# Performance work log

Measured on AMD Instinct MI355X. Metric: run time of the kernel, lower is better.

Reference implementation:

```python
import jax, jax.numpy as jnp
import numpy as np

EPS = 1e-8

def _div(n, d):
    # div_with_small_value: d = d if d > eps else eps
    return n / jnp.where(d > EPS, d, EPS)

def _lstm_dir(x, Wih, Whh, bih, bhh):
    # x: (B, L, I) -> (hs (B, L, H), h_last (B, H))
    B, L, _ = x.shape
    H = Whh.shape[1]
    xg = jnp.einsum('bli,gi->blg', x, Wih) + bih + bhh  # (B, L, 4H)
    def step(carry, g):
        h, c = carry
        g = g + h @ Whh.T
        i, f, gg, o = jnp.split(g, 4, axis=-1)
        c = jax.nn.sigmoid(f) * c + jax.nn.sigmoid(i) * jnp.tanh(gg)
        h = jax.nn.sigmoid(o) * jnp.tanh(c)
        return (h, c), h
    init = (jnp.zeros((B, H), x.dtype), jnp.zeros((B, H), x.dtype))
    (hT, _), hs = jax.lax.scan(step, init, jnp.swapaxes(xg, 0, 1))
    return jnp.swapaxes(hs, 0, 1), hT

def _bilstm(x, pf, pb):
    fw, fwT = _lstm_dir(x, *pf)
    bw_r, bwT = _lstm_dir(x[:, ::-1], *pb)
    return fw, bw_r[:, ::-1], fwT, bwT

def _mp_full(v1, v2, w):
    # v1 (B,L,H); v2 (B,H) or (B,L,H); w (P,H) -> (B,L,P)
    wv1 = v1[:, :, None, :] * w                      # (B,L,P,H)
    if v2.ndim == 2:
        wv2 = v2[:, None, None, :] * w               # (B,1,P,H)
    else:
        wv2 = v2[:, :, None, :] * w                  # (B,L,P,H)
    num = jnp.sum(wv1 * wv2, -1)
    den = jnp.linalg.norm(wv1, axis=-1) * jnp.linalg.norm(wv2, axis=-1)
    return num / jnp.maximum(den, EPS)               # torch cosine_similarity eps

def _mp_pairwise(v1, v2, w):
    # v1 (B,L1,H), v2 (B,L2,H), w (P,H) -> (B,L1,L2,P)
    wv1 = w[None, :, None, :] * v1[:, None]          # (B,P,L1,H)
    wv2 = w[None, :, None, :] * v2[:, None]          # (B,P,L2,H)
    n = jnp.einsum('bpld,bpmd->bplm', wv1, wv2)
    d = jnp.linalg.norm(wv1, axis=-1)[..., :, None] * jnp.linalg.norm(wv2, axis=-1)[..., None, :]
    return jnp.transpose(_div(n, d), (0, 2, 3, 1))

def _attention(v1, v2):
    # cosine similarity matrix (B, L1, L2)
    n = jnp.einsum('bld,bmd->blm', v1, v2)
    d = jnp.linalg.norm(v1, axis=-1)[:, :, None] * jnp.linalg.norm(v2, axis=-1)[:, None, :]
    return _div(n, d)

def _forward(emb, cWih_f, cWhh_f, cbih_f, cbhh_f, cWih_b, cWhh_b, cbih_b, cbhh_b,
             aWih_f, aWhh_f, abih_f, abhh_f, aWih_b, aWhh_b, abih_b, abhh_b,
             mp_w1, mp_w2, mp_w3, mp_w4, mp_w5, mp_w6, mp_w7, mp_w8,
             fc1_W, fc1_b, fc2_W, fc2_b, text_a, text_b):
    p = emb[text_a]
    h = emb[text_b]
    cpf_p = (cWih_f, cWhh_f, cbih_f, cbhh_f)
    cpb_p = (cWih_b, cWhh_b, cbih_b, cbhh_b)
    con_p_fw, con_p_bw, _, _ = _bilstm(p, cpf_p, cpb_p)
    con_h_fw, con_h_bw, _, _ = _bilstm(h, cpf_p, cpb_p)
    # full matching
    mv_p_full_fw = _mp_full(con_p_fw, con_h_fw[:, -1], mp_w1)
    mv_p_full_bw = _mp_full(con_p_bw, con_h_bw[:, 0], mp_w2)
    mv_h_full_fw = _mp_full(con_h_fw, con_p_fw[:, -1], mp_w1)
    mv_h_full_bw = _mp_full(con_h_bw, con_p_bw[:, 0], mp_w2)
    # maxpool matching
    mv_max_fw = _mp_pairwise(con_p_fw, con_h_fw, mp_w3)
    mv_max_bw = _mp_pairwise(con_p_bw, con_h_bw, mp_w4)
    mv_p_max_fw = mv_max_fw.max(2); mv_p_max_bw = mv_max_bw.max(2)
    mv_h_max_fw = mv_max_fw.max(1); mv_h_max_bw = mv_max_bw.max(1)
    # attentive matching
    att_fw = _attention(con_p_fw, con_h_fw)          # (B,L1,L2)
    att_bw = _attention(con_p_bw, con_h_bw)
    att_h_fw = con_h_fw[:, None] * att_fw[..., None]     # (B,L1,L2,H)
    att_h_bw = con_h_bw[:, None] * att_bw[..., None]
    att_p_fw = con_p_fw[:, :, None] * att_fw[..., None]  # (B,L1,L2,H)
    att_p_bw = con_p_bw[:, :, None] * att_bw[..., None]
    att_mean_h_fw = _div(att_h_fw.sum(2), att_fw.sum(2, keepdims=True))
    att_mean_h_bw = _div(att_h_bw.sum(2), att_bw.sum(2, keepdims=True))
    att_mean_p_fw = _div(att_p_fw.sum(1), jnp.swapaxes(att_fw.sum(1, keepdims=True), 1, 2))
    att_mean_p_bw = _div(att_p_bw.sum(1), jnp.swapaxes(att_bw.sum(1, keepdims=True), 1, 2))
    mv_p_att_mean_fw = _mp_full(con_p_fw, att_mean_h_fw, mp_w5)
    mv_p_att_mean_bw = _mp_full(con_p_bw, att_mean_h_bw, mp_w6)
    mv_h_att_mean_fw = _mp_full(con_h_fw, att_mean_p_fw, mp_w5)
    mv_h_att_mean_bw = _mp_full(con_h_bw, att_mean_p_bw, mp_w6)
    att_max_h_fw = att_h_fw.max(2); att_max_h_bw = att_h_bw.max(2)
    att_max_p_fw = att_p_fw.max(1); att_max_p_bw = att_p_bw.max(1)
    mv_p_att_max_fw = _mp_full(con_p_fw, att_max_h_fw, mp_w7)
    mv_p_att_max_bw = _mp_full(con_p_bw, att_max_h_bw, mp_w8)
    mv_h_att_max_fw = _mp_full(con_h_fw, att_max_p_fw, mp_w7)
    mv_h_att_max_bw = _mp_full(con_h_bw, att_max_p_bw, mp_w8)
    mv_p = jnp.concatenate([mv_p_full_fw, mv_p_max_fw, mv_p_att_mean_fw, mv_p_att_max_fw,
                            mv_p_full_bw, mv_p_max_bw, mv_p_att_mean_bw, mv_p_att_max_bw], 2)
    mv_h = jnp.concatenate([mv_h_full_fw, mv_h_max_fw, mv_h_att_mean_fw, mv_h_att_max_fw,
                            mv_h_full_bw, mv_h_max_bw, mv_h_att_mean_bw, mv_h_att_max_bw], 2)
    apf = (aWih_f, aWhh_f, abih_f, abhh_f)
    apb = (aWih_b, aWhh_b, abih_b, abhh_b)
    _, _, p_fwT, p_bwT = _bilstm(mv_p, apf, apb)
    _, _, h_fwT, h_bwT = _bilstm(mv_h, apf, apb)
    x = jnp.concatenate([p_fwT, p_bwT, h_fwT, h_bwT], 1)  # (B, 4H)
    x = jnp.tanh(x @ fc1_W.T + fc1_b)
    return x @ fc2_W.T + fc2_b

def setup_inputs() -> dict:
    key = jax.random.key(0)
    ks = jax.random.split(key, 40)
    B, L, V, E, H, P = 16, 128, 30000, 300, 128, 4
    def n(i, shape, s=0.05):
        return jax.random.normal(ks[i], shape, jnp.float32) * s
    inp = {
        'text_a': jax.random.randint(ks[0], (B, L), 0, V, jnp.int32),
        'text_b': jax.random.randint(ks[1], (B, L), 0, V, jnp.int32),
        'emb': n(2, (V, E), 0.1),
        'cWih_f': n(3, (4*H, E)), 'cWhh_f': n(4, (4*H, H)), 'cbih_f': n(5, (4*H,)), 'cbhh_f': n(6, (4*H,)),
        'cWih_b': n(7, (4*H, E)), 'cWhh_b': n(8, (4*H, H)), 'cbih_b': n(9, (4*H,)), 'cbhh_b': n(10, (4*H,)),
        'aWih_f': n(11, (4*H, 8*P)), 'aWhh_f': n(12, (4*H, H)), 'abih_f': n(13, (4*H,)), 'abhh_f': n(14, (4*H,)),
        'aWih_b': n(15, (4*H, 8*P)), 'aWhh_b': n(16, (4*H, H)), 'abih_b': n(17, (4*H,)), 'abhh_b': n(18, (4*H,)),
        'fc1_W': n(19, (2*H, 4*H)), 'fc1_b': n(20, (2*H,)),
        'fc2_W': n(21, (2, 2*H)), 'fc2_b': n(22, (2,)),
    }
    for i in range(1, 9):
        inp[f'mp_w{i}'] = jax.random.uniform(ks[22 + i], (P, H), jnp.float32)
    return inp

def reference(text_a, text_b, emb, cWih_f, cWhh_f, cbih_f, cbhh_f, cWih_b, cWhh_b, cbih_b, cbhh_b,
              aWih_f, aWhh_f, abih_f, abhh_f, aWih_b, aWhh_b, abih_b, abhh_b,
              fc1_W, fc1_b, fc2_W, fc2_b, mp_w1, mp_w2, mp_w3, mp_w4, mp_w5, mp_w6, mp_w7, mp_w8):
    return _forward(emb, cWih_f, cWhh_f, cbih_f, cbhh_f, cWih_b, cWhh_b, cbih_b, cbhh_b,
                    aWih_f, aWhh_f, abih_f, abhh_f, aWih_b, aWhh_b, abih_b, abhh_b,
                    mp_w1, mp_w2, mp_w3, mp_w4, mp_w5, mp_w6, mp_w7, mp_w8,
                    fc1_W, fc1_b, fc2_W, fc2_b, text_a, text_b)
```

## Files before the change

### kernel.cpp

```cpp
#include <hip/hip_runtime.h>

#define B_ 16
#define L_ 128
#define ML_ 2048
#define E_ 300
#define H_ 128
#define G_ 512
#define EPSV 1e-8f

typedef const float* fp;
typedef __attribute__((ext_vector_type(2))) float f32x2;

__device__ __forceinline__ float sigm(float x) { return 1.f / (1.f + __expf(-x)); }
__device__ __forceinline__ float tanh_f(float x) {
  float e = __expf(-2.f * fabsf(x));
  float r = (1.f - e) / (1.f + e);
  return copysignf(r, x);
}
__device__ __forceinline__ float ddiv(float n, float d) {
  return n / (d > EPSV ? d : EPSV);
}
__device__ __forceinline__ void pkfma(f32x2& d, f32x2 a, f32x2 b) {
  asm("v_pk_fma_f32 %0, %1, %2, %0" : "+v"(d) : "v"(a), "v"(b));
}

__global__ __launch_bounds__(256) void k_proj(
    fp __restrict__ emb,
    const int* __restrict__ ta, const int* __restrict__ tb,
    fp Wf, fp Wb, fp bihf, fp bhhf, fp bihb, fp bhhb,
    float* __restrict__ xg)
{
  const int z = blockIdx.z;
  const int* txt = (z >> 1) ? tb : ta;
  fp W = (z & 1) ? Wb : Wf;
  fp bih = (z & 1) ? bihb : bihf;
  fp bhh = (z & 1) ? bhhb : bhhf;
  float* out = xg + (size_t)z * ML_ * G_;
  const int m0 = blockIdx.x * 64, n0 = blockIdx.y * 64;
  __shared__ float As[12][64];
  __shared__ float Bs[12][64];
  __shared__ int rowidx[64];
  const int tid = threadIdx.x;
  if (tid < 64) rowidx[tid] = txt[m0 + tid];
  __syncthreads();
  const int tm = tid >> 4, tn = tid & 15;
  float acc[4][4] = {};
  for (int k0 = 0; k0 < 300; k0 += 12) {
    for (int i = tid; i < 768; i += 256) {
      int m = i / 12, k = i - m * 12;
      As[k][m] = emb[(size_t)rowidx[m] * 300 + k0 + k];
    }
    for (int i = tid; i < 768; i += 256) {
      int n = i / 12, k = i - n * 12;
      Bs[k][n] = W[(size_t)(n0 + n) * 300 + k0 + k];
    }
    __syncthreads();
    #pragma unroll
    for (int k = 0; k < 12; ++k) {
      float4 a = *(const float4*)&As[k][tm * 4];
      float4 bv = *(const float4*)&Bs[k][tn * 4];
      float aa[4] = {a.x, a.y, a.z, a.w};
      #pragma unroll
      for (int i = 0; i < 4; ++i) {
        acc[i][0] = fmaf(aa[i], bv.x, acc[i][0]);
        acc[i][1] = fmaf(aa[i], bv.y, acc[i][1]);
        acc[i][2] = fmaf(aa[i], bv.z, acc[i][2]);
        acc[i][3] = fmaf(aa[i], bv.w, acc[i][3]);
      }
    }
    __syncthreads();
  }
  float biasv[4];
  #pragma unroll
  for (int j = 0; j < 4; ++j)
    biasv[j] = bih[n0 + tn * 4 + j] + bhh[n0 + tn * 4 + j];
  #pragma unroll
  for (int i = 0; i < 4; ++i) {
    float* row = out + (size_t)(m0 + tm * 4 + i) * G_ + n0 + tn * 4;
    #pragma unroll
    for (int j = 0; j < 4; ++j) row[j] = acc[i][j] + biasv[j];
  }
}

__global__ __launch_bounds__(512, 2) void k_lstm(
    fp __restrict__ xg, fp Whhf, fp Whhb, float* __restrict__ out)
{
  const int b = blockIdx.x, z = blockIdx.y, dir = z & 1;
  fp Whh = dir ? Whhb : Whhf;
  fp __restrict__ xgz = xg + ((size_t)z * ML_ + (size_t)b * L_) * G_;
  float* __restrict__ outz = out + ((size_t)z * ML_ + (size_t)b * L_) * H_;
  const int tid = threadIdx.x;
  const int wv = tid >> 6, l = tid & 63;
  const int kh = l & 1, ph = (l >> 1) & 1, jj = l >> 2;
  const int j = wv * 16 + jj;
  const int rA = ph * H_ + j;
  const int rB = rA + 2 * H_;
  f32x2 wA[32], wB[32];
  {
    const float4* pA = (const float4*)(Whh + (size_t)rA * H_ + kh * 64);
    const float4* pB = (const float4*)(Whh + (size_t)rB * H_ + kh * 64);
    float4* dA = (float4*)wA; float4* dB = (float4*)wB;
    #pragma unroll
    for (int q = 0; q < 16; ++q) dA[q] = pA[q];
    #pragma unroll
    for (int q = 0; q < 16; ++q) dB[q] = pB[q];
  }
  __shared__ float hs[2][128];
  if (tid < 128) hs[0][tid] = 0.f;
  float c = 0.f;
  const int pos0 = dir ? (L_ - 1) : 0;
  float xvA = xgz[(size_t)pos0 * G_ + rA];
  float xvB = xgz[(size_t)pos0 * G_ + rB];
  __syncthreads();
  int cur = 0;
  for (int t = 0; t < L_; ++t) {
    const int pos = dir ? (L_ - 1 - t) : t;
    const int tnext = (t + 1 < L_) ? (t + 1) : t;
    const int posn = dir ? (L_ - 1 - tnext) : tnext;
    float xvA_n = xgz[(size_t)posn * G_ + rA];
    float xvB_n = xgz[(size_t)posn * G_ + rB];
    f32x2 accA0 = {0.f, 0.f}, accA1 = {0.f, 0.f};
    f32x2 accB0 = {0.f, 0.f}, accB1 = {0.f, 0.f};
    const float4* h4 = (const float4*)(&hs[cur][kh * 64]);
    #pragma unroll
    for (int q = 0; q < 16; ++q) {
      float4 hv = h4[q];
      f32x2 hlo; hlo.x = hv.x; hlo.y = hv.y;
      f32x2 hhi; hhi.x = hv.z; hhi.y = hv.w;
      pkfma(accA0, wA[2 * q],     hlo);
      pkfma(accA1, wA[2 * q + 1], hhi);
      pkfma(accB0, wB[2 * q],     hlo);
      pkfma(accB1, wB[2 * q + 1], hhi);
    }
    float aA = (accA0.x + accA0.y) + (accA1.x + accA1.y);
    float aB = (accB0.x + accB0.y) + (accB1.x + accB1.y);
    aA += __shfl_xor(aA, 1, 64);
    aB += __shfl_xor(aB, 1, 64);
    aA += xvA; aB += xvB;
    float actA = sigm(aA);
    float actB = ph ? sigm(aB) : tanh_f(aB);
    float exA = __shfl_xor(actA, 2, 64);
    float exB = __shfl_xor(actB, 2, 64);
    float iv = ph ? exA : actA;
    float fv = ph ? actA : exA;
    float gv = ph ? exB : actB;
    float ov = ph ? actB : exB;
    c = fmaf(fv, c, iv * gv);
    float hn = ov * tanh_f(c);
    const int nxt = cur ^ 1;
    if ((l & 3) == 0) {
      hs[nxt][j] = hn;
      outz[(size_t)pos * H_ + j] = hn;
    }
    asm volatile("s_waitcnt lgkmcnt(0)" ::: "memory");
    __builtin_amdgcn_s_barrier();
    cur = nxt; xvA = xvA_n; xvB = xvB_n;
  }
}

__global__ __launch_bounds__(256) void k_att(
    fp __restrict__ con, fp w3, fp w4,
    float* __restrict__ att, float* __restrict__ ameanh, float* __restrict__ amaxh,
    float* __restrict__ pcpart, float* __restrict__ mv)
{
  const int b = blockIdx.x, dir = blockIdx.y, lt = blockIdx.z;
  const int l0 = lt * 32;
  fp __restrict__ cp = con + ((size_t)dir * B_ + b) * L_ * H_;
  fp __restrict__ ch = con + ((size_t)(2 + dir) * B_ + b) * L_ * H_;
  fp w = dir ? w4 : w3;
  float* __restrict__ attg = att + ((size_t)dir * B_ + b) * L_ * L_;
  __shared__ float cps[32][132];
  __shared__ float chs[32][132];
  __shared__ float w2s[4][128];
  __shared__ float attb[32][33];
  __shared__ float pcb[4][32][33];
  __shared__ float n0l[32], nql[4][32], n0m[32], nqm[4][32], asum_s[32];
  const int tid = threadIdx.x;
  for (int i = tid; i < 512; i += 256) {
    float wv = w[i];
    w2s[i >> 7][i & 127] = wv * wv;
  }
  for (int i = tid; i < 4096; i += 256)
    cps[i >> 7][i & 127] = cp[(size_t)(l0 + (i >> 7)) * H_ + (i & 127)];
  __syncthreads();
  for (int d = tid; d < 160; d += 256) {
    int l = d / 5, q = d - l * 5;
    const float4* vr = (const float4*)&cps[l][0];
    float s = 0.f;
    if (q == 0) {
      #pragma unroll 8
      for (int h4 = 0; h4 < 32; ++h4) {
        float4 v = vr[h4];
        s += v.x*v.x + v.y*v.y + v.z*v.z + v.w*v.w;
      }
      n0l[l] = sqrtf(s);
    } else {
      const float4* wr = (const float4*)&w2s[q - 1][0];
      #pragma unroll 8
      for (int h4 = 0; h4 < 32; ++h4) {
        float4 v = vr[h4]; float4 ww = wr[h4];
        s += v.x*v.x*ww.x + v.y*v.y*ww.y + v.z*v.z*ww.z + v.w*v.w*ww.w;
      }
      nql[q - 1][l] = sqrtf(s);
    }
  }
  const int tl = tid >> 3, t8 = tid & 7;
  float amean_acc[16], amax_acc[16];
  #pragma unroll
  for (int i = 0; i < 16; ++i) { amean_acc[i] = 0.f; amax_acc[i] = -3.4e38f; }
  float asum_reg = 0.f;
  float pmax_reg = -3.4e38f;
  for (int mc = 0; mc < 4; ++mc) {
    __syncthreads();
    for (int i = tid; i < 4096; i += 256)
      chs[i >> 7][i & 127] = ch[(size_t)(mc * 32 + (i >> 7)) * H_ + (i & 127)];
    __syncthreads();
    for (int d = tid; d < 160; d += 256) {
      int m = d / 5, q = d - m * 5;
      const float4* vr = (const float4*)&chs[m][0];
      float s = 0.f;
      if (q == 0) {
        #pragma unroll 8
        for (int h4 = 0; h4 < 32; ++h4) {
          float4 v = vr[h4];
          s += v.x*v.x + v.y*v.y + v.z*v.z + v.w*v.w;
        }
        n0m[m] = sqrtf(s);
      } else {
        const float4* wr = (const float4*)&w2s[q - 1][0];
        #pragma unroll 8
        for (int h4 = 0; h4 < 32; ++h4) {
          float4 v = vr[h4]; float4 ww = wr[h4];
          s += v.x*v.x*ww.x + v.y*v.y*ww.y + v.z*v.z*ww.z + v.w*v.w*ww.w;
        }
        nqm[q - 1][m] = sqrtf(s);
      }
    }
    __syncthreads();
    float a0[4], ap0[4], ap1[4], ap2[4], ap3[4];
    #pragma unroll
    for (int mm = 0; mm < 4; ++mm) { a0[mm]=0.f; ap0[mm]=0.f; ap1[mm]=0.f; ap2[mm]=0.f; ap3[mm]=0.f; }
    #pragma unroll 4
    for (int h4 = 0; h4 < 32; ++h4) {
      const float4 av = *(const float4*)&cps[tl][h4 * 4];
      const float4 q0 = *(const float4*)&w2s[0][h4 * 4];
      const float4 q1 = *(const float4*)&w2s[1][h4 * 4];
      const float4 q2 = *(const float4*)&w2s[2][h4 * 4];
      const float4 q3 = *(const float4*)&w2s[3][h4 * 4];
      #pragma unroll
      for (int mm = 0; mm < 4; ++mm) {
        const float4 cv = *(const float4*)&chs[t8 * 4 + mm][h4 * 4];
        float px = av.x * cv.x, py = av.y * cv.y, pz = av.z * cv.z, pw = av.w * cv.w;
        a0[mm] += (px + py) + (pz + pw);
        ap0[mm] += px * q0.x + py * q0.y + pz * q0.z + pw * q0.w;
        ap1[mm] += px * q1.x + py * q1.y + pz * q1.z + pw * q1.w;
        ap2[mm] += px * q2.x + py * q2.y + pz * q2.z + pw * q2.w;
        ap3[mm] += px * q3.x + py * q3.y + pz * q3.z + pw * q3.w;
      }
    }
    #pragma unroll
    for (int mm = 0; mm < 4; ++mm) {
      const int m = t8 * 4 + mm;
      float attv = ddiv(a0[mm], n0l[tl] * n0m[m]);
      attb[tl][m] = attv;
      attg[(size_t)(l0 + tl) * L_ + mc * 32 + m] = attv;
      pcb[0][tl][m] = ddiv(ap0[mm], nql[0][tl] * nqm[0][m]);
      pcb[1][tl][m] = ddiv(ap1[mm], nql[1][tl] * nqm[1][m]);
      pcb[2][tl][m] = ddiv(ap2[mm], nql[2][tl] * nqm[2][m]);
      pcb[3][tl][m] = ddiv(ap3[mm], nql[3][tl] * nqm[3][m]);
    }
    __syncthreads();
    for (int mq = 0; mq < 32; ++mq) {
      float avv = attb[tl][mq];
      const float4* cr = (const float4*)&chs[mq][t8 * 16];
      #pragma unroll
      for (int i = 0; i < 4; ++i) {
        float4 cv = cr[i];
        float t0 = avv * cv.x, t1 = avv * cv.y, t2 = avv * cv.z, t3 = avv * cv.w;
        amean_acc[4*i+0] += t0; amax_acc[4*i+0] = fmaxf(amax_acc[4*i+0], t0);
        amean_acc[4*i+1] += t1; amax_acc[4*i+1] = fmaxf(amax_acc[4*i+1], t1);
        amean_acc[4*i+2] += t2; amax_acc[4*i+2] = fmaxf(amax_acc[4*i+2], t2);
        amean_acc[4*i+3] += t3; amax_acc[4*i+3] = fmaxf(amax_acc[4*i+3], t3);
      }
    }
    if (tid < 32) {
      float s = 0.f;
      for (int mq = 0; mq < 32; ++mq) s += attb[tid][mq];
      asum_reg += s;
    }
    if (tid < 128) {
      const int p = tid >> 5, q = tid & 31;
      float mx = pmax_reg;
      for (int mq = 0; mq < 32; ++mq) mx = fmaxf(mx, pcb[p][q][mq]);
      pmax_reg = mx;
      float mx2 = -3.4e38f;
      for (int lq = 0; lq < 32; ++lq) mx2 = fmaxf(mx2, pcb[p][lq][q]);
      pcpart[((((size_t)dir * B_ + b) * 4 + lt) * 4 + p) * L_ + mc * 32 + q] = mx2;
    }
    __syncthreads();
  }
  if (tid < 32) asum_s[tid] = asum_reg;
  __syncthreads();
  {
    float den = asum_s[tl]; den = (den > EPSV) ? den : EPSV;
    const size_t base = (((size_t)dir * B_ + b) * L_ + l0 + tl) * H_ + t8 * 16;
    #pragma unroll
    for (int i = 0; i < 16; ++i) {
      ameanh[base + i] = amean_acc[i] / den;
      amaxh[base + i] = amax_acc[i];
    }
  }
  if (tid < 128) {
    const int p = tid >> 5, lq = tid & 31;
    mv[(size_t)(b * L_ + l0 + lq) * 32 + (dir ? 20 : 4) + p] = pmax_reg;
  }
}

__global__ __launch_bounds__(256) void k_col(
    fp __restrict__ con, fp __restrict__ att,
    fp __restrict__ pcpart,
    float* __restrict__ ameanp, float* __restrict__ amaxp, float* __restrict__ mv)
{
  const int b = blockIdx.x, dir = blockIdx.y, mt = blockIdx.z;
  const int m0 = mt * 32;
  fp __restrict__ cp = con + ((size_t)dir * B_ + b) * L_ * H_;
  fp __restrict__ attg = att + ((size_t)dir * B_ + b) * L_ * L_;
  __shared__ float atts[128][33];
  __shared__ float cpc[32][132];
  __shared__ float asum_s[32];
  const int tid = threadIdx.x;
  for (int i = tid; i < 4096; i += 256)
    atts[i >> 5][i & 31] = attg[(size_t)(i >> 5) * L_ + m0 + (i & 31)];
  __syncthreads();
  if (tid < 32) {
    float s = 0.f;
    for (int l = 0; l < 128; ++l) s += atts[l][tid];
    asum_s[tid] = s;
  }
  const int tm = tid >> 3, t8 = tid & 7;
  float mean_acc[16], max_acc[16];
  #pragma unroll
  for (int i = 0; i < 16; ++i) { mean_acc[i] = 0.f; max_acc[i] = -3.4e38f; }
  for (int lc = 0; lc < 4; ++lc) {
    __syncthreads();
    for (int i = tid; i < 4096; i += 256)
      cpc[i >> 7][i & 127] = cp[(size_t)(lc * 32 + (i >> 7)) * H_ + (i & 127)];
    __syncthreads();
    for (int lq = 0; lq < 32; ++lq) {
      float avv = atts[lc * 32 + lq][tm];
      const float4* cr = (const float4*)&cpc[lq][t8 * 16];
      #pragma unroll
      for (int i = 0; i < 4; ++i) {
        float4 cv = cr[i];
        float t0 = avv * cv.x, t1 = avv * cv.y, t2 = avv * cv.z, t3 = avv * cv.w;
        mean_acc[4*i+0] += t0; max_acc[4*i+0] = fmaxf(max_acc[4*i+0], t0);
        mean_acc[4*i+1] += t1; max_acc[4*i+1] = fmaxf(max_acc[4*i+1], t1);
        mean_acc[4*i+2] += t2; max_acc[4*i+2] = fmaxf(max_acc[4*i+2], t2);
        mean_acc[4*i+3] += t3; max_acc[4*i+3] = fmaxf(max_acc[4*i+3], t3);
      }
    }
  }
  __syncthreads();
  {
    float den = asum_s[tm]; den = (den > EPSV) ? den : EPSV;
    const size_t base = (((size_t)dir * B_ + b) * L_ + m0 + tm) * H_ + t8 * 16;
    #pragma unroll
    for (int i = 0; i < 16; ++i) {
      ameanp[base + i] = mean_acc[i] / den;
      amaxp[base + i] = max_acc[i];
    }
  }
  if (tid < 128) {
    const int p = tid >> 5, mq = tid & 31;
    float mx = -3.4e38f;
    #pragma unroll
    for (int lt = 0; lt < 4; ++lt)
      mx = fmaxf(mx, pcpart[((((size_t)dir * B_ + b) * 4 + lt) * 4 + p) * L_ + m0 + mq]);
    mv[(size_t)(ML_ + b * L_ + m0 + mq) * 32 + (dir ? 20 : 4) + p] = mx;
  }
}

__global__ __launch_bounds__(256) void k_mv(
    fp __restrict__ con,
    fp __restrict__ ameanh, fp __restrict__ amaxh,
    fp __restrict__ ameanp, fp __restrict__ amaxp,
    fp w1, fp w2, fp w5, fp w6, fp w7, fp w8,
    float* __restrict__ mv)
{
  int idx = blockIdx.x * 256 + threadIdx.x;
  const int p = idx & 3; int t1 = idx >> 2;
  const int type = t1 % 3; int t2 = t1 / 3;
  const int dir = t2 & 1; int t3 = t2 >> 1;
  const int l = t3 & 127; int t4 = t3 >> 7;
  const int b = t4 & 15; const int side = t4 >> 4;
  const float* v1 = con + (((size_t)(side ? 2 : 0) + dir) * B_ + b) * L_ * H_ + (size_t)l * H_;
  const float* v2;
  if (type == 0) {
    v2 = con + (((size_t)(side ? 0 : 2) + dir) * B_ + b) * L_ * H_ + (size_t)(dir ? 0 : L_ - 1) * H_;
  } else {
    const float* base = (type == 1) ? (side ? ameanp : ameanh) : (side ? amaxp : amaxh);
    v2 = base + (((size_t)dir * B_ + b) * L_ + l) * H_;
  }
  fp w = (type == 0) ? (dir ? w2 : w1) : (type == 1) ? (dir ? w6 : w5) : (dir ? w8 : w7);
  w += p * H_;
  float num = 0.f, s1 = 0.f, s2 = 0.f;
  for (int h = 0; h < H_; ++h) {
    float wv = w[h];
    float a = v1[h] * wv, bb = v2[h] * wv;
    num = fmaf(a, bb, num);
    s1 = fmaf(a, a, s1);
    s2 = fmaf(bb, bb, s2);
  }
  float den = sqrtf(s1) * sqrtf(s2);
  int slot = (type == 0) ? (dir ? 16 : 0) + p : (type == 1) ? (dir ? 24 : 8) + p : (dir ? 28 : 12) + p;
  mv[((size_t)side * ML_ + b * L_ + l) * 32 + slot] = ddiv(num, den);
}

__global__ __launch_bounds__(256) void k_aggproj(
    fp __restrict__ mv,
    fp Wf, fp Wb, fp bihf, fp bhhf, fp bihb, fp bhhb,
    float* __restrict__ xg)
{
  const int z = blockIdx.y, side = z >> 1, dir = z & 1;
  fp W = dir ? Wb : Wf;
  fp bih = dir ? bihb : bihf;
  fp bhh = dir ? bhhb : bhhf;
  const int r0 = blockIdx.x * 8;
  const float* src = mv + ((size_t)side * ML_ + r0) * 32;
  float* out = xg + ((size_t)z * ML_ + r0) * G_;
  __shared__ float mvs[8][32];
  const int tid = threadIdx.x;
  mvs[tid >> 5][tid & 31] = src[tid];
  __syncthreads();
  float w0[32], w1v[32];
  {
    const float4* wp = (const float4*)(W + (size_t)tid * 32);
    #pragma unroll
    for (int q = 0; q < 8; ++q) {
      float4 u = wp[q];
      w0[4*q+0] = u.x; w0[4*q+1] = u.y; w0[4*q+2] = u.z; w0[4*q+3] = u.w;
    }
    const float4* wp2 = (const float4*)(W + (size_t)(tid + 256) * 32);
    #pragma unroll
    for (int q = 0; q < 8; ++q) {
      float4 u = wp2[q];
      w1v[4*q+0] = u.x; w1v[4*q+1] = u.y; w1v[4*q+2] = u.z; w1v[4*q+3] = u.w;
    }
  }
  float bias0 = bih[tid] + bhh[tid];
  float bias1 = bih[tid + 256] + bhh[tid + 256];
  for (int r = 0; r < 8; ++r) {
    float acc0 = bias0, acc1 = bias1;
    #pragma unroll
    for (int k = 0; k < 32; ++k) {
      float xv = mvs[r][k];
      acc0 = fmaf(w0[k], xv, acc0);
      acc1 = fmaf(w1v[k], xv, acc1);
    }
    out[(size_t)r * G_ + tid] = acc0;
    out[(size_t)r * G_ + tid + 256] = acc1;
  }
}

__global__ __launch_bounds__(256) void k_fc(
    fp __restrict__ aggseq,
    fp fc1W, fp fc1b, fp fc2W, fp fc2b,
    float* __restrict__ out)
{
  const int b = blockIdx.x, tid = threadIdx.x;
  __shared__ float x[512];
  __shared__ float y[256];
  for (int i = tid; i < 512; i += 256) {
    int z = i >> 7, h = i & 127;
    int l = (z & 1) ? 0 : (L_ - 1);
    x[i] = aggseq[(((size_t)z * B_ + b) * L_ + l) * H_ + h];
  }
  __syncthreads();
  {
    float acc = fc1b[tid];
    const float4* wr = (const float4*)(fc1W + (size_t)tid * 512);
    const float4* x4 = (const float4*)x;
    #pragma unroll 8
    for (int k4 = 0; k4 < 128; ++k4) {
      float4 u = wr[k4];
      float4 xv = x4[k4];
      acc = fmaf(u.x, xv.x, acc);
      acc = fmaf(u.y, xv.y, acc);
      acc = fmaf(u.z, xv.z, acc);
      acc = fmaf(u.w, xv.w, acc);
    }
    y[tid] = tanh_f(acc);
  }
  __syncthreads();
  if (tid < 2) {
    float acc = fc2b[tid];
    for (int k = 0; k < 256; ++k) acc = fmaf(fc2W[tid * 256 + k], y[k], acc);
    out[b * 2 + tid] = acc;
  }
}

extern "C" void kernel_launch(void* const* d_in, const int* in_sizes, int n_in,
                              void* d_out, int out_size, void* d_ws, size_t ws_size,
                              hipStream_t stream) {
  (void)in_sizes; (void)n_in; (void)out_size; (void)ws_size;
  const int* ta = (const int*)d_in[0];
  const int* tb = (const int*)d_in[1];
  fp emb   = (fp)d_in[2];
  fp cWihf = (fp)d_in[3];
  fp cWhhf = (fp)d_in[4];
  fp cbihf = (fp)d_in[5];
  fp cbhhf = (fp)d_in[6];
  fp cWihb = (fp)d_in[7];
  fp cWhhb = (fp)d_in[8];
  fp cbihb = (fp)d_in[9];
  fp cbhhb = (fp)d_in[10];
  fp aWihf = (fp)d_in[11];
  fp aWhhf = (fp)d_in[12];
  fp abihf = (fp)d_in[13];
  fp abhhf = (fp)d_in[14];
  fp aWihb = (fp)d_in[15];
  fp aWhhb = (fp)d_in[16];
  fp abihb = (fp)d_in[17];
  fp abhhb = (fp)d_in[18];
  fp fc1W  = (fp)d_in[19];
  fp fc1b  = (fp)d_in[20];
  fp fc2W  = (fp)d_in[21];
  fp fc2b  = (fp)d_in[22];
  fp w1 = (fp)d_in[23];
  fp w2 = (fp)d_in[24];
  fp w3 = (fp)d_in[25];
  fp w4 = (fp)d_in[26];
  fp w5 = (fp)d_in[27];
  fp w6 = (fp)d_in[28];
  fp w7 = (fp)d_in[29];
  fp w8 = (fp)d_in[30];

  float* ws = (float*)d_ws;
  float* xg     = ws;
  float* con    = xg     + (size_t)4 * ML_ * G_;
  float* attw   = con    + (size_t)4 * ML_ * H_;
  float* ameanh = attw   + (size_t)2 * B_ * L_ * L_;
  float* amaxh  = ameanh + (size_t)2 * ML_ * H_;
  float* ameanp = amaxh  + (size_t)2 * ML_ * H_;
  float* amaxp  = ameanp + (size_t)2 * ML_ * H_;
  float* pcpart = amaxp  + (size_t)2 * ML_ * H_;
  float* mvb    = pcpart + (size_t)2 * B_ * 16 * L_;
  float* aggseq = mvb    + (size_t)2 * ML_ * 32;

  k_proj<<<dim3(32, 8, 4), 256, 0, stream>>>(emb, ta, tb, cWihf, cWihb,
                                             cbihf, cbhhf, cbihb, cbhhb, xg);
  k_lstm<<<dim3(16, 4), 512, 0, stream>>>(xg, cWhhf, cWhhb, con);
  k_att<<<dim3(16, 2, 4), 256, 0, stream>>>(con, w3, w4, attw, ameanh, amaxh, pcpart, mvb);
  k_col<<<dim3(16, 2, 4), 256, 0, stream>>>(con, attw, pcpart, ameanp, amaxp, mvb);
  k_mv<<<384, 256, 0, stream>>>(con, ameanh, amaxh, ameanp, amaxp, w1, w2, w5, w6, w7, w8, mvb);
  k_aggproj<<<dim3(256, 4), 256, 0, stream>>>(mvb, aWihf, aWihb, abihf, abhhf, abihb, abhhb, xg);
  k_lstm<<<dim3(16, 4), 512, 0, stream>>>(xg, aWhhf, aWhhb, aggseq);
  k_fc<<<16, 256, 0, stream>>>(aggseq, fc1W, fc1b, fc2W, fc2b, (float*)d_out);
}
```

Measured before the change: 503.5 us.

## Split LSTM recurrent matvec four ways over K with butterfly reduce-scatter

Reassigns work in the recurrent LSTM kernel so each lane of a 4-lane group holds all four gates for one hidden unit over a 32-wide K slice, replacing the old 2-way K split with 2 gates per lane. Partial sums are combined with a reduce-scatter using shuffles, so each lane computes one gate activation, and gates are then exchanged with further shuffles. The goal is to halve the LDS h reads per lane and shorten the per-step serial FMA chain. The cost is more cross-lane shuffles and select logic on the critical path of every timestep.

```diff
diff --git a/kernel.cpp b/kernel.cpp
--- a/kernel.cpp
+++ b/kernel.cpp
@@ -91,70 +91,78 @@
   float* __restrict__ outz = out + ((size_t)z * ML_ + (size_t)b * L_) * H_;
   const int tid = threadIdx.x;
   const int wv = tid >> 6, l = tid & 63;
-  const int kh = l & 1, ph = (l >> 1) & 1, jj = l >> 2;
-  const int j = wv * 16 + jj;
-  const int rA = ph * H_ + j;
-  const int rB = rA + 2 * H_;
-  f32x2 wA[32], wB[32];
-  {
-    const float4* pA = (const float4*)(Whh + (size_t)rA * H_ + kh * 64);
-    const float4* pB = (const float4*)(Whh + (size_t)rB * H_ + kh * 64);
-    float4* dA = (float4*)wA; float4* dB = (float4*)wB;
-    #pragma unroll
-    for (int q = 0; q < 16; ++q) dA[q] = pA[q];
-    #pragma unroll
-    for (int q = 0; q < 16; ++q) dB[q] = pB[q];
+  const int kh = l & 3, rg = l >> 2;
+  const int j = wv * 16 + rg;
+  const int b0 = kh & 1, b1 = (kh >> 1) & 1;
+  float4 wq[4][8];
+  #pragma unroll
+  for (int g = 0; g < 4; ++g) {
+    const float4* p = (const float4*)(Whh + (size_t)(g * 128 + j) * H_ + kh * 32);
+    #pragma unroll
+    for (int q = 0; q < 8; ++q) wq[g][q] = p[q];
   }
   __shared__ float hs[2][128];
   if (tid < 128) hs[0][tid] = 0.f;
   float c = 0.f;
   const int pos0 = dir ? (L_ - 1) : 0;
-  float xvA = xgz[(size_t)pos0 * G_ + rA];
-  float xvB = xgz[(size_t)pos0 * G_ + rB];
+  float xv = xgz[(size_t)pos0 * G_ + kh * 128 + j];
   __syncthreads();
   int cur = 0;
   for (int t = 0; t < L_; ++t) {
     const int pos = dir ? (L_ - 1 - t) : t;
-    const int tnext = (t + 1 < L_) ? (t + 1) : t;
-    const int posn = dir ? (L_ - 1 - tnext) : tnext;
-    float xvA_n = xgz[(size_t)posn * G_ + rA];
-    float xvB_n = xgz[(size_t)posn * G_ + rB];
-    f32x2 accA0 = {0.f, 0.f}, accA1 = {0.f, 0.f};
-    f32x2 accB0 = {0.f, 0.f}, accB1 = {0.f, 0.f};
-    const float4* h4 = (const float4*)(&hs[cur][kh * 64]);
-    #pragma unroll
-    for (int q = 0; q < 16; ++q) {
+    const int tnx = (t + 1 < L_) ? (t + 1) : t;
+    const int posn = dir ? (L_ - 1 - tnx) : tnx;
+    float xvn = xgz[(size_t)posn * G_ + kh * 128 + j];
+    f32x2 a2[4];
+    #pragma unroll
+    for (int g = 0; g < 4; ++g) { a2[g].x = 0.f; a2[g].y = 0.f; }
+    const float4* h4 = (const float4*)(&hs[cur][kh * 32]);
+    #pragma unroll
+    for (int q = 0; q < 8; ++q) {
       float4 hv = h4[q];
       f32x2 hlo; hlo.x = hv.x; hlo.y = hv.y;
       f32x2 hhi; hhi.x = hv.z; hhi.y = hv.w;
-      pkfma(accA0, wA[2 * q],     hlo);
-      pkfma(accA1, wA[2 * q + 1], hhi);
-      pkfma(accB0, wB[2 * q],     hlo);
-      pkfma(accB1, wB[2 * q + 1], hhi);
-    }
-    float aA = (accA0.x + accA0.y) + (accA1.x + accA1.y);
-    float aB = (accB0.x + accB0.y) + (accB1.x + accB1.y);
-    aA += __shfl_xor(aA, 1, 64);
-    aB += __shfl_xor(aB, 1, 64);
-    aA += xvA; aB += xvB;
-    float actA = sigm(aA);
-    float actB = ph ? sigm(aB) : tanh_f(aB);
-    float exA = __shfl_xor(actA, 2, 64);
-    float exB = __shfl_xor(actB, 2, 64);
-    float iv = ph ? exA : actA;
-    float fv = ph ? actA : exA;
-    float gv = ph ? exB : actB;
-    float ov = ph ? actB : exB;
+      #pragma unroll
+      for (int g = 0; g < 4; ++g) {
+        float4 wqv = wq[g][q];
+        f32x2 wlo; wlo.x = wqv.x; wlo.y = wqv.y;
+        f32x2 whi; whi.x = wqv.z; whi.y = wqv.w;
+        pkfma(a2[g], wlo, hlo);
+        pkfma(a2[g], whi, hhi);
+      }
+    }
+    float pg0 = a2[0].x + a2[0].y;
+    float pg1 = a2[1].x + a2[1].y;
+    float pg2 = a2[2].x + a2[2].y;
+    float pg3 = a2[3].x + a2[3].y;
+    float sendA = b0 ? pg0 : pg1;
+    float sendB = b0 ? pg2 : pg3;
+    float keepA = b0 ? pg1 : pg0;
+    float keepB = b0 ? pg3 : pg2;
+    float uA = keepA + __shfl_xor(sendA, 1, 64);
+    float uB = keepB + __shfl_xor(sendB, 1, 64);
+    float mine  = b1 ? uB : uA;
+    float send2 = b1 ? uA : uB;
+    float tot = mine + __shfl_xor(send2, 2, 64);
+    float pre = tot + xv;
+    float act = (kh == 2) ? tanh_f(pre) : sigm(pre);
+    float e1 = __shfl_xor(act, 1, 64);
+    float e2 = __shfl_xor(act, 2, 64);
+    float e3 = __shfl_xor(e1, 2, 64);
+    float iv = (kh == 0) ? act : (kh == 1) ? e1 : (kh == 2) ? e2 : e3;
+    float fv = (kh == 0) ? e1 : (kh == 1) ? act : (kh == 2) ? e3 : e2;
+    float gv = (kh == 0) ? e2 : (kh == 1) ? e3 : (kh == 2) ? act : e1;
+    float ov = (kh == 0) ? e3 : (kh == 1) ? e2 : (kh == 2) ? e1 : act;
     c = fmaf(fv, c, iv * gv);
     float hn = ov * tanh_f(c);
     const int nxt = cur ^ 1;
-    if ((l & 3) == 0) {
+    if (kh == 0) {
       hs[nxt][j] = hn;
       outz[(size_t)pos * H_ + j] = hn;
     }
     asm volatile("s_waitcnt lgkmcnt(0)" ::: "memory");
     __builtin_amdgcn_s_barrier();
-    cur = nxt; xvA = xvA_n; xvB = xvB_n;
+    cur = nxt; xv = xvn;
   }
 }
 
```

After: 479.5 us. -4.8%, faster.

## Split LSTM recurrent dot products across four lanes with 1024-thread blocks

Applied to the files above, without the earlier changes.

The recurrent LSTM kernel now runs 1024 threads per block. Each gate row's 128-wide dot product is split over four lanes of 32 elements each instead of two lanes of 64, which halves the serial FMA chain and the register-held weights per thread. The shared hidden-state buffer is padded (36-float stride per quarter) to avoid LDS bank conflicts on the vector reads. In exchange the kernel needs an extra shuffle-reduction stage and a barrier across 16 waves each timestep, which may add synchronisation latency on the sequential critical path.

```diff
diff --git a/kernel.cpp b/kernel.cpp
--- a/kernel.cpp
+++ b/kernel.cpp
@@ -10,6 +10,7 @@
 
 typedef const float* fp;
 typedef __attribute__((ext_vector_type(2))) float f32x2;
+typedef __attribute__((ext_vector_type(4))) float f32x4;
 
 __device__ __forceinline__ float sigm(float x) { return 1.f / (1.f + __expf(-x)); }
 __device__ __forceinline__ float tanh_f(float x) {
@@ -82,7 +83,7 @@
   }
 }
 
-__global__ __launch_bounds__(512, 2) void k_lstm(
+__global__ __launch_bounds__(1024, 4) void k_lstm(
     fp __restrict__ xg, fp Whhf, fp Whhb, float* __restrict__ out)
 {
   const int b = blockIdx.x, z = blockIdx.y, dir = z & 1;
@@ -90,57 +91,67 @@
   fp __restrict__ xgz = xg + ((size_t)z * ML_ + (size_t)b * L_) * G_;
   float* __restrict__ outz = out + ((size_t)z * ML_ + (size_t)b * L_) * H_;
   const int tid = threadIdx.x;
-  const int wv = tid >> 6, l = tid & 63;
-  const int kh = l & 1, ph = (l >> 1) & 1, jj = l >> 2;
-  const int j = wv * 16 + jj;
+  const int j = tid >> 3, kh = tid & 3, ph = (tid >> 2) & 1;
   const int rA = ph * H_ + j;
   const int rB = rA + 2 * H_;
-  f32x2 wA[32], wB[32];
+  f32x4 wA[8], wB[8];
   {
-    const float4* pA = (const float4*)(Whh + (size_t)rA * H_ + kh * 64);
-    const float4* pB = (const float4*)(Whh + (size_t)rB * H_ + kh * 64);
-    float4* dA = (float4*)wA; float4* dB = (float4*)wB;
-    #pragma unroll
-    for (int q = 0; q < 16; ++q) dA[q] = pA[q];
-    #pragma unroll
-    for (int q = 0; q < 16; ++q) dB[q] = pB[q];
-  }
-  __shared__ float hs[2][128];
-  if (tid < 128) hs[0][tid] = 0.f;
+    const f32x4* pA = (const f32x4*)(Whh + (size_t)rA * H_ + kh * 32);
+    const f32x4* pB = (const f32x4*)(Whh + (size_t)rB * H_ + kh * 32);
+    #pragma unroll
+    for (int q = 0; q < 8; ++q) wA[q] = pA[q];
+    #pragma unroll
+    for (int q = 0; q < 8; ++q) wB[q] = pB[q];
+  }
+  __shared__ float hs[2][144];
+  if (tid < 144) hs[0][tid] = 0.f;
   float c = 0.f;
   const int pos0 = dir ? (L_ - 1) : 0;
-  float xvA = xgz[(size_t)pos0 * G_ + rA];
-  float xvB = xgz[(size_t)pos0 * G_ + rB];
+  float xvA = 0.f, xvB = 0.f;
+  if (kh == 0) {
+    xvA = xgz[(size_t)pos0 * G_ + rA];
+    xvB = xgz[(size_t)pos0 * G_ + rB];
+  }
   __syncthreads();
   int cur = 0;
   for (int t = 0; t < L_; ++t) {
     const int pos = dir ? (L_ - 1 - t) : t;
-    const int tnext = (t + 1 < L_) ? (t + 1) : t;
-    const int posn = dir ? (L_ - 1 - tnext) : tnext;
-    float xvA_n = xgz[(size_t)posn * G_ + rA];
-    float xvB_n = xgz[(size_t)posn * G_ + rB];
-    f32x2 accA0 = {0.f, 0.f}, accA1 = {0.f, 0.f};
-    f32x2 accB0 = {0.f, 0.f}, accB1 = {0.f, 0.f};
-    const float4* h4 = (const float4*)(&hs[cur][kh * 64]);
-    #pragma unroll
-    for (int q = 0; q < 16; ++q) {
-      float4 hv = h4[q];
+    const int tnx = (t + 1 < L_) ? (t + 1) : t;
+    const int posn = dir ? (L_ - 1 - tnx) : tnx;
+    float xvA_n = 0.f, xvB_n = 0.f;
+    if (kh == 0) {
+      xvA_n = xgz[(size_t)posn * G_ + rA];
+      xvB_n = xgz[(size_t)posn * G_ + rB];
+    }
+    f32x2 aA0 = {0.f, 0.f}, aA1 = {0.f, 0.f};
+    f32x2 aB0 = {0.f, 0.f}, aB1 = {0.f, 0.f};
+    const f32x4* h4 = (const f32x4*)(&hs[cur][kh * 36]);
+    #pragma unroll
+    for (int q = 0; q < 8; ++q) {
+      f32x4 hv = h4[q];
       f32x2 hlo; hlo.x = hv.x; hlo.y = hv.y;
       f32x2 hhi; hhi.x = hv.z; hhi.y = hv.w;
-      pkfma(accA0, wA[2 * q],     hlo);
-      pkfma(accA1, wA[2 * q + 1], hhi);
-      pkfma(accB0, wB[2 * q],     hlo);
-      pkfma(accB1, wB[2 * q + 1], hhi);
-    }
-    float aA = (accA0.x + accA0.y) + (accA1.x + accA1.y);
-    float aB = (accB0.x + accB0.y) + (accB1.x + accB1.y);
-    aA += __shfl_xor(aA, 1, 64);
-    aB += __shfl_xor(aB, 1, 64);
-    aA += xvA; aB += xvB;
-    float actA = sigm(aA);
-    float actB = ph ? sigm(aB) : tanh_f(aB);
-    float exA = __shfl_xor(actA, 2, 64);
-    float exB = __shfl_xor(actB, 2, 64);
+      f32x4 wa = wA[q];
+      f32x2 walo; walo.x = wa.x; walo.y = wa.y;
+      f32x2 wahi; wahi.x = wa.z; wahi.y = wa.w;
+      pkfma(aA0, walo, hlo);
+      pkfma(aA1, wahi, hhi);
+      f32x4 wb = wB[q];
+      f32x2 wblo; wblo.x = wb.x; wblo.y = wb.y;
+      f32x2 wbhi; wbhi.x = wb.z; wbhi.y = wb.w;
+      pkfma(aB0, wblo, hlo);
+      pkfma(aB1, wbhi, hhi);
+    }
+    float pA = (aA0.x + aA0.y) + (aA1.x + aA1.y) + xvA;
+    float pB = (aB0.x + aB0.y) + (aB1.x + aB1.y) + xvB;
+    pA += __shfl_xor(pA, 1, 64);
+    pB += __shfl_xor(pB, 1, 64);
+    pA += __shfl_xor(pA, 2, 64);
+    pB += __shfl_xor(pB, 2, 64);
+    float actA = sigm(pA);
+    float actB = ph ? sigm(pB) : tanh_f(pB);
+    float exA = __shfl_xor(actA, 4, 64);
+    float exB = __shfl_xor(actB, 4, 64);
     float iv = ph ? exA : actA;
     float fv = ph ? actA : exA;
     float gv = ph ? exB : actB;
@@ -148,8 +159,8 @@
     c = fmaf(fv, c, iv * gv);
     float hn = ov * tanh_f(c);
     const int nxt = cur ^ 1;
-    if ((l & 3) == 0) {
-      hs[nxt][j] = hn;
+    if ((tid & 7) == 0) {
+      hs[nxt][(j >> 5) * 36 + (j & 31)] = hn;
       outz[(size_t)pos * H_ + j] = hn;
     }
     asm volatile("s_waitcnt lgkmcnt(0)" ::: "memory");
@@ -549,11 +560,11 @@
 
   k_proj<<<dim3(32, 8, 4), 256, 0, stream>>>(emb, ta, tb, cWihf, cWihb,
                                              cbihf, cbhhf, cbihb, cbhhb, xg);
-  k_lstm<<<dim3(16, 4), 512, 0, stream>>>(xg, cWhhf, cWhhb, con);
+  k_lstm<<<dim3(16, 4), 1024, 0, stream>>>(xg, cWhhf, cWhhb, con);
   k_att<<<dim3(16, 2, 4), 256, 0, stream>>>(con, w3, w4, attw, ameanh, amaxh, pcpart, mvb);
   k_col<<<dim3(16, 2, 4), 256, 0, stream>>>(con, attw, pcpart, ameanp, amaxp, mvb);
   k_mv<<<384, 256, 0, stream>>>(con, ameanh, amaxh, ameanp, amaxp, w1, w2, w5, w6, w7, w8, mvb);
   k_aggproj<<<dim3(256, 4), 256, 0, stream>>>(mvb, aWihf, aWihb, abihf, abhhf, abihb, abhhb, xg);
-  k_lstm<<<dim3(16, 4), 512, 0, stream>>>(xg, aWhhf, aWhhb, aggseq);
+  k_lstm<<<dim3(16, 4), 1024, 0, stream>>>(xg, aWhhf, aWhhb, aggseq);
   k_fc<<<16, 256, 0, stream>>>(aggseq, fc1W, fc1b, fc2W, fc2b, (float*)d_out);
 }
```

New measurement: 572.8 us. +13.8%, slower.
